# Kernel optimization log

Hardware: AMD Instinct MI355X
Metric: run time of the kernel (lower is better)

Reference implementation:

```python
import jax, jax.numpy as jnp
import numpy as np

K = 7          # local attention kernel size
PAD = 3        # (K-1)//2 so output spatial dims match input
GROUPS = 8

def unfold2d(x, k):
    # x: [B, C, H+k-1, W+k-1] -> patches [B, C, H, W, k*k] (kh-major, kw-minor, matching F.unfold)
    B, C, Hp, Wp = x.shape
    H, W = Hp - k + 1, Wp - k + 1
    return jnp.stack([x[:, :, i:i + H, j:j + W] for i in range(k) for j in range(k)], axis=-1)

def setup_inputs():
    key = jax.random.key(0)
    k1, k2, k3, k4, k5, k6 = jax.random.split(key, 6)
    B, Cin, H, W = 2, 256, 56, 56
    outc = 256
    scale = (2.0 / Cin) ** 0.5  # kaiming fan_out-ish init
    return {
        "feature_map": jax.random.normal(k1, (B, 2 * Cin, H, W), jnp.float32),
        "w_q": jax.random.normal(k2, (outc, Cin), jnp.float32) * scale,
        "w_k": jax.random.normal(k3, (outc, Cin), jnp.float32) * scale,
        "w_v": jax.random.normal(k4, (outc, Cin), jnp.float32) * scale,
        "rel_h": jax.random.normal(k5, (outc // 2, K), jnp.float32),
        "rel_w": jax.random.normal(k6, (outc // 2, K), jnp.float32),
    }

def reference(feature_map, w_q, w_k, w_v, rel_h, rel_w):
    B, C2, H, W = feature_map.shape
    Cin = C2 // 2
    fm_t0, fm_t1 = feature_map[:, :Cin], feature_map[:, Cin:]
    outc = w_q.shape[0]
    # 1x1 convs (bias=False)
    q = jnp.einsum('oc,bchw->bohw', w_q, fm_t1)                      # [B, outc, H, W]
    padded = jnp.pad(fm_t0, ((0, 0), (0, 0), (PAD, PAD), (PAD, PAD)))
    kk = jnp.einsum('oc,bchw->bohw', w_k, padded)
    vv = jnp.einsum('oc,bchw->bohw', w_v, padded)
    k_out = unfold2d(kk, K)                                          # [B, outc, H, W, K*K]
    v_out = unfold2d(vv, K)
    # relative position bias: first half channels get row bias, second half col bias
    half = outc // 2
    bias_h = jnp.broadcast_to(rel_h[:, :, None], (half, K, K)).reshape(half, K * K)
    bias_w = jnp.broadcast_to(rel_w[:, None, :], (half, K, K)).reshape(half, K * K)
    bias = jnp.concatenate([bias_h, bias_w], axis=0)                 # [outc, K*K]
    k_out = k_out + bias[None, :, None, None, :]
    G, Cg = GROUPS, outc // GROUPS
    qg = q.reshape(B, G, Cg, H, W)
    kg = k_out.reshape(B, G, Cg, H, W, K * K)
    vg = v_out.reshape(B, G, Cg, H, W, K * K)
    logits = jnp.einsum('bgchw,bgchwk->bghwk', qg, kg)
    wts = jax.nn.softmax(logits, axis=-1)
    out = jnp.einsum('bghwk,bgchwk->bgchw', wts, vg)
    return out.reshape(B, outc, H, W)
```

## Files before the change

kernel.cpp:

```cpp
#include <hip/hip_runtime.h>
#include <hip/hip_bf16.h>

#define B    2
#define CIN  256
#define H    56
#define W    56
#define OUTC 256
#define KS   7
#define PAD  3
#define G    8
#define CG   32
#define HP   62
#define WP   62
#define P1   (H * W)
#define P2   (HP * WP)

typedef __attribute__((ext_vector_type(2))) _Float16 h2;
typedef __attribute__((ext_vector_type(8))) _Float16 f16x8;
typedef __attribute__((ext_vector_type(8))) unsigned short ushort8;
typedef __attribute__((ext_vector_type(4))) float f32x4;

__device__ inline unsigned short f2h(float f) {
    const _Float16 h = (_Float16)f;
    return *(const unsigned short*)&h;
}

__device__ inline float fdot2(h2 a, h2 b, float c) {
#if defined(__has_builtin)
#if __has_builtin(__builtin_amdgcn_fdot2)
    return __builtin_amdgcn_fdot2(a, b, c, false);
#else
    return c + (float)a[0] * (float)b[0] + (float)a[1] * (float)b[1];
#endif
#else
    return c + (float)a[0] * (float)b[0] + (float)a[1] * (float)b[1];
#endif
}

__device__ inline float dot8(const f16x8 q, const f16x8 k, float s) {
    s = fdot2((h2){q[0], q[1]}, (h2){k[0], k[1]}, s);
    s = fdot2((h2){q[2], q[3]}, (h2){k[2], k[3]}, s);
    s = fdot2((h2){q[4], q[5]}, (h2){k[4], k[5]}, s);
    s = fdot2((h2){q[6], q[7]}, (h2){k[6], k[7]}, s);
    return s;
}

#define ASTR 40
__global__ __launch_bounds__(256, 2) void gemm_kernel(const float* __restrict__ fm,
                                                      const float* __restrict__ wq,
                                                      const float* __restrict__ wk,
                                                      const float* __restrict__ wv,
                                                      unsigned short* __restrict__ qi,
                                                      unsigned short* __restrict__ ki,
                                                      unsigned short* __restrict__ vi) {
    const int b = blockIdx.z;
    const bool isQ = blockIdx.y < 2;
    if (isQ && blockIdx.x >= 25) return;
    const int o0 = (isQ ? blockIdx.y : (blockIdx.y - 2)) * 128;
    const int n0 = blockIdx.x * 128;
    const int Nreal = isQ ? P1 : P2;
    const int Pstr  = isQ ? P1 : P2;

    const float* Wsrc;
    int orow0;
    if (isQ)            { Wsrc = wq; orow0 = o0; }
    else if (o0 < 256)  { Wsrc = wk; orow0 = o0; }
    else                { Wsrc = wv; orow0 = o0 - 256; }

    __shared__ unsigned short Alds[128 * ASTR];
    __shared__ unsigned short Blds[128 * ASTR];
    const int tid = threadIdx.x;
    const int lane = tid & 63;
    const int wave = tid >> 6;
    const int wr = (wave >> 1) * 64;
    const int wc = (wave & 1) * 64;
    const int lrow = lane & 15;
    const int quad = lane >> 4;

    const int arow = tid & 127;
    const int akc  = (tid >> 7) * 16;

    const int n = n0 + arow;
    int srcoff = -1;
    if (isQ) {
        if (n < P1) srcoff = n;
    } else {
        if (n < P2) {
            const int y = n / WP, x = n - y * WP;
            const int iy = y - PAD, ix = x - PAD;
            if (iy >= 0 && iy < H && ix >= 0 && ix < W) srcoff = iy * W + ix;
        }
    }
    const float* fmB = fm + ((size_t)b * (2 * CIN) + (isQ ? CIN : 0)) * P1;
    const float* wrow = Wsrc + (size_t)orow0 * CIN + (size_t)arow * CIN + akc;

    unsigned short* alp = Alds + arow * ASTR + akc;
    unsigned short* blp = Blds + arow * ASTR + akc;

    f32x4 acc[4][4] = {};

    float av[16], bv[16];
    {
        const float4 a0 = ((const float4*)wrow)[0];
        const float4 a1 = ((const float4*)wrow)[1];
        const float4 a2 = ((const float4*)wrow)[2];
        const float4 a3 = ((const float4*)wrow)[3];
        av[0]=a0.x; av[1]=a0.y; av[2]=a0.z; av[3]=a0.w;
        av[4]=a1.x; av[5]=a1.y; av[6]=a1.z; av[7]=a1.w;
        av[8]=a2.x; av[9]=a2.y; av[10]=a2.z; av[11]=a2.w;
        av[12]=a3.x; av[13]=a3.y; av[14]=a3.z; av[15]=a3.w;
        #pragma unroll
        for (int j = 0; j < 16; ++j)
            bv[j] = (srcoff >= 0) ? fmB[(size_t)(akc + j) * P1 + srcoff] : 0.f;
    }

    for (int kb = 0; kb < CIN / 32; ++kb) {
        {
            f16x8 p0, p1, p2, p3;
            #pragma unroll
            for (int j = 0; j < 8; ++j) {
                p0[j] = (_Float16)av[j];
                p1[j] = (_Float16)av[8 + j];
                p2[j] = (_Float16)bv[j];
                p3[j] = (_Float16)bv[8 + j];
            }
            *(f16x8*)(alp)     = p0;
            *(f16x8*)(alp + 8) = p1;
            *(f16x8*)(blp)     = p2;
            *(f16x8*)(blp + 8) = p3;
        }
        __syncthreads();
        if (kb < CIN / 32 - 1) {
            const int c0 = (kb + 1) * 32 + akc;
            const float* wnext = wrow + (kb + 1) * 32;
            const float4 a0 = ((const float4*)wnext)[0];
            const float4 a1 = ((const float4*)wnext)[1];
            const float4 a2 = ((const float4*)wnext)[2];
            const float4 a3 = ((const float4*)wnext)[3];
            av[0]=a0.x; av[1]=a0.y; av[2]=a0.z; av[3]=a0.w;
            av[4]=a1.x; av[5]=a1.y; av[6]=a1.z; av[7]=a1.w;
            av[8]=a2.x; av[9]=a2.y; av[10]=a2.z; av[11]=a2.w;
            av[12]=a3.x; av[13]=a3.y; av[14]=a3.z; av[15]=a3.w;
            #pragma unroll
            for (int j = 0; j < 16; ++j)
                bv[j] = (srcoff >= 0) ? fmB[(size_t)(c0 + j) * P1 + srcoff] : 0.f;
        }
        f16x8 af[4], bfr[4];
        #pragma unroll
        for (int mi = 0; mi < 4; ++mi)
            af[mi] = *(const f16x8*)&Alds[(wr + mi * 16 + lrow) * ASTR + quad * 8];
        #pragma unroll
        for (int ni = 0; ni < 4; ++ni)
            bfr[ni] = *(const f16x8*)&Blds[(wc + ni * 16 + lrow) * ASTR + quad * 8];
        #pragma unroll
        for (int mi = 0; mi < 4; ++mi)
            #pragma unroll
            for (int ni = 0; ni < 4; ++ni)
                acc[mi][ni] = __builtin_amdgcn_mfma_f32_16x16x32_f16(af[mi], bfr[ni], acc[mi][ni], 0, 0, 0);
        __syncthreads();
    }

    #pragma unroll
    for (int mi = 0; mi < 4; ++mi) {
        const int gmBase = o0 + wr + mi * 16 + quad * 4;
        int ch0;
        unsigned short* base;
        if (isQ)               { ch0 = gmBase;       base = qi; }
        else if (gmBase < 256) { ch0 = gmBase;       base = ki; }
        else                   { ch0 = gmBase - 256; base = vi; }
        const int g   = ch0 >> 5;
        const int sub = (ch0 >> 3) & 3;
        const int l8  = ch0 & 7;
        unsigned short* pbase = base + ((((size_t)b * 8 + g) * 4 + sub) * Pstr) * 8 + l8;
        #pragma unroll
        for (int ni = 0; ni < 4; ++ni) {
            const int gn = n0 + wc + ni * 16 + lrow;
            if (gn < Nreal) {
                ushort4 pk;
                pk.x = f2h(acc[mi][ni][0]);
                pk.y = f2h(acc[mi][ni][1]);
                pk.z = f2h(acc[mi][ni][2]);
                pk.w = f2h(acc[mi][ni][3]);
                *(ushort4*)(pbase + (size_t)gn * 8) = pk;
            }
        }
    }
}

__global__ __launch_bounds__(256) void attn_kernel(const unsigned short* __restrict__ qi,
                                                   const unsigned short* __restrict__ ki,
                                                   const unsigned short* __restrict__ vi,
                                                   const float* __restrict__ rel_h,
                                                   const float* __restrict__ rel_w,
                                                   float* __restrict__ out) {
    const int b = blockIdx.z;
    const int g = blockIdx.y;
    const int tid = threadIdx.x;

    int p = blockIdx.x * 256 + tid;
    const bool act = p < P1;
    if (!act) p = P1 - 1;

    const int h = p / W;
    const int w = p - h * W;
    const int pos0 = h * WP + w;
    const size_t bg4 = ((size_t)b * G + g) * 4;

    f16x8 qh[4];
    #pragma unroll
    for (int s = 0; s < 4; ++s)
        qh[s] = *(const f16x8*)(qi + ((bg4 + s) * P1 + p) * 8);

    const float* rel = (g < 4) ? (rel_h + (size_t)g * CG * KS)
                               : (rel_w + (size_t)(g - 4) * CG * KS);
    float bd[KS];
    #pragma unroll
    for (int t = 0; t < KS; ++t) {
        float s0 = 0.f;
        #pragma unroll
        for (int s = 0; s < 4; ++s)
            #pragma unroll
            for (int j = 0; j < 8; ++j)
                s0 += (float)qh[s][j] * rel[(s * 8 + j) * KS + t];
        bd[t] = s0;
    }

    float logits[KS * KS];
    #pragma unroll
    for (int i = 0; i < KS; ++i)
        #pragma unroll
        for (int j = 0; j < KS; ++j)
            logits[i * KS + j] = (g < 4) ? bd[i] : bd[j];

    #pragma unroll
    for (int s = 0; s < 4; ++s) {
        const unsigned short* kp = ki + ((bg4 + s) * P2 + pos0) * 8;
        const f16x8 q = qh[s];
        #pragma unroll
        for (int i = 0; i < KS; ++i) {
            const unsigned short* kr = kp + i * WP * 8;
            #pragma unroll
            for (int j = 0; j < KS; ++j) {
                const f16x8 kv = *(const f16x8*)(kr + j * 8);
                logits[i * KS + j] = dot8(q, kv, logits[i * KS + j]);
            }
        }
    }

    {
        float m = logits[0];
        #pragma unroll
        for (int t = 1; t < KS * KS; ++t) m = fmaxf(m, logits[t]);
        float sum = 0.f;
        #pragma unroll
        for (int t = 0; t < KS * KS; ++t) {
            const float e = __expf(logits[t] - m);
            logits[t] = e;
            sum += e;
        }
        const float inv = 1.f / sum;
        #pragma unroll
        for (int t = 0; t < KS * KS; ++t) logits[t] *= inv;
    }

    #pragma unroll
    for (int s = 0; s < 4; ++s) {
        const unsigned short* vp = vi + ((bg4 + s) * P2 + pos0) * 8;
        float a[8] = {};
        #pragma unroll
        for (int i = 0; i < KS; ++i) {
            const unsigned short* vr = vp + i * WP * 8;
            #pragma unroll
            for (int j = 0; j < KS; ++j) {
                const f16x8 vv = *(const f16x8*)(vr + j * 8);
                const float wt = logits[i * KS + j];
                #pragma unroll
                for (int c = 0; c < 8; ++c)
                    a[c] += wt * (float)vv[c];
            }
        }
        if (act) {
            float* op = out + ((size_t)b * OUTC + g * CG + s * 8) * P1 + p;
            #pragma unroll
            for (int c = 0; c < 8; ++c)
                op[(size_t)c * P1] = a[c];
        }
    }
}

extern "C" void kernel_launch(void* const* d_in, const int* in_sizes, int n_in,
                              void* d_out, int out_size, void* d_ws, size_t ws_size,
                              hipStream_t stream) {
    const float* fm = (const float*)d_in[0];
    const float* wq = (const float*)d_in[1];
    const float* wk = (const float*)d_in[2];
    const float* wv = (const float*)d_in[3];
    const float* rh = (const float*)d_in[4];
    const float* rw = (const float*)d_in[5];
    float* out = (float*)d_out;

    unsigned short* ws = (unsigned short*)d_ws;
    unsigned short* qi = ws;
    unsigned short* ki = qi + (size_t)B * OUTC * P1;
    unsigned short* vi = ki + (size_t)B * OUTC * P2;

    gemm_kernel<<<dim3(31, 6, B), 256, 0, stream>>>(fm, wq, wk, wv, qi, ki, vi);
    attn_kernel<<<dim3((P1 + 255) / 256, G, B), 256, 0, stream>>>(qi, ki, vi, rh, rw, out);
}
```

Measured before the change: 114.3 us.

## Split attention channel-subgroups across 4 lanes with shuffle-reduced logits

Each pixel is now handled by four adjacent threads, each owning one 8-channel slice of the 32-channel group. Partial logits (including the relative-position bias term) are summed across the four lanes with xor shuffles, and then each lane runs the softmax and its own slice of the value aggregation. This gives four times as many threads and lowers per-thread register pressure for better occupancy and latency hiding. The cost is 98 shuffles per thread and softmax work repeated in every lane. The bounds check is dropped because P1*4 is an exact multiple of 256.

```diff
diff --git a/kernel.cpp b/kernel.cpp
--- a/kernel.cpp
+++ b/kernel.cpp
@@ -195,34 +195,27 @@
                                                    float* __restrict__ out) {
     const int b = blockIdx.z;
     const int g = blockIdx.y;
-    const int tid = threadIdx.x;
-
-    int p = blockIdx.x * 256 + tid;
-    const bool act = p < P1;
-    if (!act) p = P1 - 1;
+    const int t = blockIdx.x * 256 + threadIdx.x;
+    const int s = t & 3;
+    const int p = t >> 2;
 
     const int h = p / W;
     const int w = p - h * W;
     const int pos0 = h * WP + w;
-    const size_t bg4 = ((size_t)b * G + g) * 4;
-
-    f16x8 qh[4];
-    #pragma unroll
-    for (int s = 0; s < 4; ++s)
-        qh[s] = *(const f16x8*)(qi + ((bg4 + s) * P1 + p) * 8);
+    const size_t plane = ((size_t)b * G + g) * 4 + s;
+
+    const f16x8 q = *(const f16x8*)(qi + (plane * P1 + p) * 8);
 
     const float* rel = (g < 4) ? (rel_h + (size_t)g * CG * KS)
                                : (rel_w + (size_t)(g - 4) * CG * KS);
     float bd[KS];
     #pragma unroll
-    for (int t = 0; t < KS; ++t) {
+    for (int t7 = 0; t7 < KS; ++t7) {
         float s0 = 0.f;
         #pragma unroll
-        for (int s = 0; s < 4; ++s)
-            #pragma unroll
-            for (int j = 0; j < 8; ++j)
-                s0 += (float)qh[s][j] * rel[(s * 8 + j) * KS + t];
-        bd[t] = s0;
+        for (int j = 0; j < 8; ++j)
+            s0 += (float)q[j] * rel[(s * 8 + j) * KS + t7];
+        bd[t7] = s0;
     }
 
     float logits[KS * KS];
@@ -232,10 +225,8 @@
         for (int j = 0; j < KS; ++j)
             logits[i * KS + j] = (g < 4) ? bd[i] : bd[j];
 
-    #pragma unroll
-    for (int s = 0; s < 4; ++s) {
-        const unsigned short* kp = ki + ((bg4 + s) * P2 + pos0) * 8;
-        const f16x8 q = qh[s];
+    {
+        const unsigned short* kp = ki + (plane * P2 + pos0) * 8;
         #pragma unroll
         for (int i = 0; i < KS; ++i) {
             const unsigned short* kr = kp + i * WP * 8;
@@ -247,25 +238,32 @@
         }
     }
 
+    #pragma unroll
+    for (int t49 = 0; t49 < KS * KS; ++t49) {
+        float v = logits[t49];
+        v += __shfl_xor(v, 1);
+        v += __shfl_xor(v, 2);
+        logits[t49] = v;
+    }
+
     {
         float m = logits[0];
         #pragma unroll
-        for (int t = 1; t < KS * KS; ++t) m = fmaxf(m, logits[t]);
+        for (int t49 = 1; t49 < KS * KS; ++t49) m = fmaxf(m, logits[t49]);
         float sum = 0.f;
         #pragma unroll
-        for (int t = 0; t < KS * KS; ++t) {
-            const float e = __expf(logits[t] - m);
-            logits[t] = e;
+        for (int t49 = 0; t49 < KS * KS; ++t49) {
+            const float e = __expf(logits[t49] - m);
+            logits[t49] = e;
             sum += e;
         }
         const float inv = 1.f / sum;
         #pragma unroll
-        for (int t = 0; t < KS * KS; ++t) logits[t] *= inv;
-    }
-
-    #pragma unroll
-    for (int s = 0; s < 4; ++s) {
-        const unsigned short* vp = vi + ((bg4 + s) * P2 + pos0) * 8;
+        for (int t49 = 0; t49 < KS * KS; ++t49) logits[t49] *= inv;
+    }
+
+    {
+        const unsigned short* vp = vi + (plane * P2 + pos0) * 8;
         float a[8] = {};
         #pragma unroll
         for (int i = 0; i < KS; ++i) {
@@ -279,12 +277,10 @@
                     a[c] += wt * (float)vv[c];
             }
         }
-        if (act) {
-            float* op = out + ((size_t)b * OUTC + g * CG + s * 8) * P1 + p;
-            #pragma unroll
-            for (int c = 0; c < 8; ++c)
-                op[(size_t)c * P1] = a[c];
-        }
+        float* op = out + ((size_t)b * OUTC + g * CG + s * 8) * P1 + p;
+        #pragma unroll
+        for (int c = 0; c < 8; ++c)
+            op[(size_t)c * P1] = a[c];
     }
 }
 
@@ -305,5 +301,5 @@
     unsigned short* vi = ki + (size_t)B * OUTC * P2;
 
     gemm_kernel<<<dim3(31, 6, B), 256, 0, stream>>>(fm, wq, wk, wv, qi, ki, vi);
-    attn_kernel<<<dim3((P1 + 255) / 256, G, B), 256, 0, stream>>>(qi, ki, vi, rh, rw, out);
-}
+    attn_kernel<<<dim3(P1 * 4 / 256, G, B), 256, 0, stream>>>(qi, ki, vi, rh, rw, out);
+}
```

After: 122.2 us. 1.07x slower.
